# Kernel tuning notes

Hardware: AMD Instinct MI355X
Metric: run time of the kernel (lower is better)

The kernel has to match this reference:

```python
import jax, jax.numpy as jnp
import numpy as np

B, T, H, UNITS = 32, 2048, 1024, 1024
NEG_BIG = -1e9

def setup_inputs() -> dict:
    key = jax.random.key(0)
    k1, k2, k3, k4 = jax.random.split(key, 4)
    enc_hs = jax.random.normal(k1, (B, T, H), dtype=jnp.float32)
    dec_ht = jax.random.normal(k2, (B, H), dtype=jnp.float32)
    mask = jax.random.randint(k3, (B, T), 0, 2).astype(jnp.bool_)
    # Dense(units, use_bias=False) kernel: (H, UNITS), he_normal-like scale
    Wa = jax.random.normal(k4, (H, UNITS), dtype=jnp.float32) * np.sqrt(2.0 / H)
    return {"enc_hs": enc_hs, "dec_ht": dec_ht, "mask": mask, "Wa": Wa}

def reference(enc_hs, dec_ht, mask, Wa):
    # mask-apply on encoder states: (B,T,H) * (B,T,1)
    enc = enc_hs * mask[:, :, None].astype(enc_hs.dtype)
    # 'general' score: dec_ht @ (enc @ Wa)^T  -> (B,T)
    proj = jnp.einsum('bth,hu->btu', enc, Wa)           # (B,T,UNITS)
    score = jnp.einsum('bh,bth->bt', dec_ht, proj)      # (B,T)
    # additive mask: where mask is False, add -1e9
    score = score + (~mask).astype(score.dtype) * NEG_BIG
    attn = jax.nn.softmax(score, axis=-1)               # (B,T)
    # context = attn-weighted sum of masked encoder states -> (B,H)
    context = jnp.einsum('bt,bth->bh', attn, enc)
    return context
```

## Files before the change

kernel.cpp:

```cpp
#include <hip/hip_runtime.h>
#include <math.h>
#include <cstdint>
#include <cstddef>

#define BB 32
#define TT 2048
#define HH 1024
#define UU 1024
#define NC 64
#define CT 32
#define NEG_BIG (-1e9f)

__global__ __launch_bounds__(256) void k_v(const float* __restrict__ Wa,
                                           const float* __restrict__ dec,
                                           float* __restrict__ v) {
    __shared__ float lds[4 * UU];
    const int tid = threadIdx.x;
    const int h0  = blockIdx.x * 4;

    const float4* Wa4  = reinterpret_cast<const float4*>(Wa + (size_t)h0 * UU);
    float4*       lds4 = reinterpret_cast<float4*>(lds);
    #pragma unroll
    for (int i = 0; i < 4; ++i)
        lds4[i * 256 + tid] = Wa4[i * 256 + tid];
    __syncthreads();

    const int wid = tid >> 6, lane = tid & 63;
    for (int j = 0; j < 8; ++j) {
        const int b = wid * 8 + j;
        const float4* d4 = reinterpret_cast<const float4*>(dec + (size_t)b * UU);
        float4 dreg[4];
        #pragma unroll
        for (int k = 0; k < 4; ++k) dreg[k] = d4[k * 64 + lane];

        float p[4];
        #pragma unroll
        for (int r = 0; r < 4; ++r) {
            float acc = 0.f;
            #pragma unroll
            for (int k = 0; k < 4; ++k) {
                const float4 a = lds4[r * 256 + k * 64 + lane];
                acc += a.x * dreg[k].x + a.y * dreg[k].y +
                       a.z * dreg[k].z + a.w * dreg[k].w;
            }
            p[r] = acc;
        }
        #pragma unroll
        for (int r = 0; r < 4; ++r) {
            #pragma unroll
            for (int off = 32; off > 0; off >>= 1)
                p[r] += __shfl_xor(p[r], off, 64);
        }
        if (lane == 0) {
            #pragma unroll
            for (int r = 0; r < 4; ++r)
                v[(size_t)b * HH + h0 + r] = p[r];
        }
    }
}

__global__ __launch_bounds__(256) void k_flash(const float* __restrict__ enc,
                                               const int* __restrict__ mask,
                                               const float* __restrict__ v,
                                               float* __restrict__ pm,
                                               float* __restrict__ pl,
                                               float* __restrict__ pctx) {
    const int tid  = threadIdx.x;
    const int wid  = tid >> 6, lane = tid & 63;
    const int w    = blockIdx.x * 4 + wid;
    const int b    = w / NC;
    const int c    = w % NC;
    const int t0   = c * CT;

    const float4* v4 = reinterpret_cast<const float4*>(v + (size_t)b * HH);
    float4 vr[4];
    #pragma unroll
    for (int k = 0; k < 4; ++k) vr[k] = v4[k * 64 + lane];

    float m = -INFINITY, l = 0.f;
    float4 ctx[4];
    #pragma unroll
    for (int k = 0; k < 4; ++k) ctx[k] = make_float4(0.f, 0.f, 0.f, 0.f);

    const int*    mrow = mask + (size_t)b * TT + t0;
    const float4* erow = reinterpret_cast<const float4*>(
                             enc + ((size_t)b * TT + t0) * HH);

    #pragma unroll 4
    for (int t = 0; t < CT; ++t) {
        float4 e[4];
        #pragma unroll
        for (int k = 0; k < 4; ++k)
            e[k] = erow[(size_t)t * 256 + k * 64 + lane];

        float p = 0.f;
        #pragma unroll
        for (int k = 0; k < 4; ++k)
            p += e[k].x * vr[k].x + e[k].y * vr[k].y +
                 e[k].z * vr[k].z + e[k].w * vr[k].w;
        #pragma unroll
        for (int off = 32; off > 0; off >>= 1)
            p += __shfl_xor(p, off, 64);

        const int   mv   = mrow[t];
        const float s    = mv ? p : NEG_BIG;
        const float keep = mv ? 1.f : 0.f;

        const float mnew  = fmaxf(m, s);
        const float alpha = __expf(m - mnew);
        const float pe    = __expf(s - mnew);
        l = l * alpha + pe;
        const float pk = pe * keep;
        #pragma unroll
        for (int k = 0; k < 4; ++k) {
            ctx[k].x = ctx[k].x * alpha + pk * e[k].x;
            ctx[k].y = ctx[k].y * alpha + pk * e[k].y;
            ctx[k].z = ctx[k].z * alpha + pk * e[k].z;
            ctx[k].w = ctx[k].w * alpha + pk * e[k].w;
        }
        m = mnew;
    }

    if (lane == 0) { pm[w] = m; pl[w] = l; }
    float4* p4 = reinterpret_cast<float4*>(pctx + (size_t)w * HH);
    #pragma unroll
    for (int k = 0; k < 4; ++k) p4[k * 64 + lane] = ctx[k];
}

__global__ __launch_bounds__(256) void k_reduce(const float* __restrict__ pm,
                                                const float* __restrict__ pl,
                                                const float* __restrict__ pctx,
                                                float* __restrict__ out) {
    const int b = blockIdx.x;
    const int h = blockIdx.y * 256 + threadIdx.x;
    __shared__ float wsh[NC];

    float M = -INFINITY;
    for (int c = 0; c < NC; ++c) M = fmaxf(M, pm[b * NC + c]);
    float L = 0.f;
    for (int c = 0; c < NC; ++c) L += pl[b * NC + c] * __expf(pm[b * NC + c] - M);

    if (threadIdx.x < NC)
        wsh[threadIdx.x] = __expf(pm[b * NC + threadIdx.x] - M);
    __syncthreads();

    float acc = 0.f;
    for (int c = 0; c < NC; ++c)
        acc += wsh[c] * pctx[((size_t)b * NC + c) * HH + h];

    out[(size_t)b * HH + h] = acc / L;
}

extern "C" void kernel_launch(void* const* d_in, const int* in_sizes, int n_in,
                              void* d_out, int out_size, void* d_ws, size_t ws_size,
                              hipStream_t stream) {
    const float* enc  = (const float*)d_in[0];
    const float* dec  = (const float*)d_in[1];
    const int*   mask = (const int*)  d_in[2];
    const float* Wa   = (const float*)d_in[3];
    float*       out  = (float*)d_out;

    float* ws   = (float*)d_ws;
    float* v    = ws;
    float* pm   = v  + (size_t)BB * HH;
    float* pl   = pm + (size_t)BB * NC;
    float* pctx = pl + (size_t)BB * NC;

    k_v<<<HH / 4, 256, 0, stream>>>(Wa, dec, v);
    k_flash<<<(BB * NC) / 4, 256, 0, stream>>>(enc, mask, v, pm, pl, pctx);
    dim3 g2(BB, HH / 256);
    k_reduce<<<g2, 256, 0, stream>>>(pm, pl, pctx, out);
}
```

Before: 385.0 us.

## Skip loading masked encoder rows and split sequence into more chunks

New measurement: 360.8 us. 1.07x faster.

```diff
diff --git a/kernel.cpp b/kernel.cpp
--- a/kernel.cpp
+++ b/kernel.cpp
@@ -7,8 +7,8 @@
 #define TT 2048
 #define HH 1024
 #define UU 1024
-#define NC 64
-#define CT 32
+#define NCH 128
+#define CT 16
 #define NEG_BIG (-1e9f)
 
 __global__ __launch_bounds__(256) void k_v(const float* __restrict__ Wa,
@@ -59,17 +59,17 @@
     }
 }
 
-__global__ __launch_bounds__(256) void k_flash(const float* __restrict__ enc,
-                                               const int* __restrict__ mask,
-                                               const float* __restrict__ v,
-                                               float* __restrict__ pm,
-                                               float* __restrict__ pl,
-                                               float* __restrict__ pctx) {
+__global__ __launch_bounds__(256, 4) void k_flash(const float* __restrict__ enc,
+                                                  const int* __restrict__ mask,
+                                                  const float* __restrict__ v,
+                                                  float* __restrict__ pm,
+                                                  float* __restrict__ pl,
+                                                  float* __restrict__ pctx) {
     const int tid  = threadIdx.x;
     const int wid  = tid >> 6, lane = tid & 63;
     const int w    = blockIdx.x * 4 + wid;
-    const int b    = w / NC;
-    const int c    = w % NC;
+    const int b    = w >> 7;
+    const int c    = w & (NCH - 1);
     const int t0   = c * CT;
 
     const float4* v4 = reinterpret_cast<const float4*>(v + (size_t)b * HH);
@@ -77,48 +77,54 @@
     #pragma unroll
     for (int k = 0; k < 4; ++k) vr[k] = v4[k * 64 + lane];
 
+    const int* mrow = mask + (size_t)b * TT + t0;
+    int mv[CT];
+    #pragma unroll
+    for (int t = 0; t < CT; ++t) mv[t] = mrow[t];
+
     float m = -INFINITY, l = 0.f;
     float4 ctx[4];
     #pragma unroll
     for (int k = 0; k < 4; ++k) ctx[k] = make_float4(0.f, 0.f, 0.f, 0.f);
 
-    const int*    mrow = mask + (size_t)b * TT + t0;
     const float4* erow = reinterpret_cast<const float4*>(
                              enc + ((size_t)b * TT + t0) * HH);
 
     #pragma unroll 4
     for (int t = 0; t < CT; ++t) {
-        float4 e[4];
-        #pragma unroll
-        for (int k = 0; k < 4; ++k)
-            e[k] = erow[(size_t)t * 256 + k * 64 + lane];
+        if (mv[t]) {
+            float4 e[4];
+            #pragma unroll
+            for (int k = 0; k < 4; ++k)
+                e[k] = erow[(size_t)t * 256 + k * 64 + lane];
 
-        float p = 0.f;
-        #pragma unroll
-        for (int k = 0; k < 4; ++k)
-            p += e[k].x * vr[k].x + e[k].y * vr[k].y +
-                 e[k].z * vr[k].z + e[k].w * vr[k].w;
-        #pragma unroll
-        for (int off = 32; off > 0; off >>= 1)
-            p += __shfl_xor(p, off, 64);
+            float p = 0.f;
+            #pragma unroll
+            for (int k = 0; k < 4; ++k)
+                p += e[k].x * vr[k].x + e[k].y * vr[k].y +
+                     e[k].z * vr[k].z + e[k].w * vr[k].w;
+            #pragma unroll
+            for (int off = 32; off > 0; off >>= 1)
+                p += __shfl_xor(p, off, 64);
 
-        const int   mv   = mrow[t];
-        const float s    = mv ? p : NEG_BIG;
-        const float keep = mv ? 1.f : 0.f;
-
-        const float mnew  = fmaxf(m, s);
-        const float alpha = __expf(m - mnew);
-        const float pe    = __expf(s - mnew);
-        l = l * alpha + pe;
-        const float pk = pe * keep;
-        #pragma unroll
-        for (int k = 0; k < 4; ++k) {
-            ctx[k].x = ctx[k].x * alpha + pk * e[k].x;
-            ctx[k].y = ctx[k].y * alpha + pk * e[k].y;
-            ctx[k].z = ctx[k].z * alpha + pk * e[k].z;
-            ctx[k].w = ctx[k].w * alpha + pk * e[k].w;
+            const float mnew  = fmaxf(m, p);
+            const float alpha = __expf(m - mnew);
+            const float pe    = __expf(p - mnew);
+            l = l * alpha + pe;
+            #pragma unroll
+            for (int k = 0; k < 4; ++k) {
+                ctx[k].x = ctx[k].x * alpha + pe * e[k].x;
+                ctx[k].y = ctx[k].y * alpha + pe * e[k].y;
+                ctx[k].z = ctx[k].z * alpha + pe * e[k].z;
+                ctx[k].w = ctx[k].w * alpha + pe * e[k].w;
+            }
+            m = mnew;
+        } else {
+            const float mnew  = fmaxf(m, NEG_BIG);
+            const float alpha = __expf(m - mnew);
+            l = l * alpha + __expf(NEG_BIG - mnew);
+            m = mnew;
         }
-        m = mnew;
     }
 
     if (lane == 0) { pm[w] = m; pl[w] = l; }
@@ -133,20 +139,25 @@
                                                 float* __restrict__ out) {
     const int b = blockIdx.x;
     const int h = blockIdx.y * 256 + threadIdx.x;
-    __shared__ float wsh[NC];
+    __shared__ float sm[NCH], sl[NCH];
+
+    if (threadIdx.x < NCH) {
+        sm[threadIdx.x] = pm[b * NCH + threadIdx.x];
+        sl[threadIdx.x] = pl[b * NCH + threadIdx.x];
+    }
+    __syncthreads();
 
     float M = -INFINITY;
-    for (int c = 0; c < NC; ++c) M = fmaxf(M, pm[b * NC + c]);
+    #pragma unroll 8
+    for (int c = 0; c < NCH; ++c) M = fmaxf(M, sm[c]);
     float L = 0.f;
-    for (int c = 0; c < NC; ++c) L += pl[b * NC + c] * __expf(pm[b * NC + c] - M);
-
-    if (threadIdx.x < NC)
-        wsh[threadIdx.x] = __expf(pm[b * NC + threadIdx.x] - M);
-    __syncthreads();
+    #pragma unroll 8
+    for (int c = 0; c < NCH; ++c) L += sl[c] * __expf(sm[c] - M);
 
     float acc = 0.f;
-    for (int c = 0; c < NC; ++c)
-        acc += wsh[c] * pctx[((size_t)b * NC + c) * HH + h];
+    #pragma unroll 8
+    for (int c = 0; c < NCH; ++c)
+        acc += __expf(sm[c] - M) * pctx[((size_t)b * NCH + c) * HH + h];
 
     out[(size_t)b * HH + h] = acc / L;
 }
@@ -163,11 +174,11 @@
     float* ws   = (float*)d_ws;
     float* v    = ws;
     float* pm   = v  + (size_t)BB * HH;
-    float* pl   = pm + (size_t)BB * NC;
-    float* pctx = pl + (size_t)BB * NC;
+    float* pl   = pm + (size_t)BB * NCH;
+    float* pctx = pl + (size_t)BB * NCH;
 
     k_v<<<HH / 4, 256, 0, stream>>>(Wa, dec, v);
-    k_flash<<<(BB * NC) / 4, 256, 0, stream>>>(enc, mask, v, pm, pl, pctx);
+    k_flash<<<(BB * NCH) / 4, 256, 0, stream>>>(enc, mask, v, pm, pl, pctx);
     dim3 g2(BB, HH / 256);
     k_reduce<<<g2, 256, 0, stream>>>(pm, pl, pctx, out);
 }
```
